# Kernel tuning notes

Measured on AMD Instinct MI355X. Metric: run time of the kernel, lower is better.

## Reference

```python
import jax, jax.numpy as jnp
import numpy as np

CHUNK = 128


def setup_inputs() -> dict:
    key = jax.random.key(0)
    ks = jax.random.split(key, 10)
    B, L, d, n = 4, 2048, 192, 64
    sd = 1.0 / np.sqrt(d)
    return {
        "x": jax.random.normal(ks[0], (B, L, d), dtype=jnp.float32),
        "A_log": -jnp.log(2.0) + 0.1 * jax.random.normal(ks[1], (d,), dtype=jnp.float32),
        "W_B": sd * jax.random.normal(ks[2], (n, d), dtype=jnp.float32),
        "W_C": sd * jax.random.normal(ks[3], (n, d), dtype=jnp.float32),
        "W_dt": sd * jax.random.normal(ks[4], (d, d), dtype=jnp.float32),
        "b_dt": 0.1 * jax.random.normal(ks[5], (d,), dtype=jnp.float32),
        "W_xp": sd * jax.random.normal(ks[6], (2 * d, d), dtype=jnp.float32),
        "b_xp": 0.1 * jax.random.normal(ks[7], (2 * d,), dtype=jnp.float32),
        "W_out": sd * jax.random.normal(ks[8], (d, d), dtype=jnp.float32),
        "b_out": 0.1 * jax.random.normal(ks[9], (d,), dtype=jnp.float32),
    }


def reference(x, A_log, W_B, W_C, W_dt, b_dt, W_xp, b_xp, W_out, b_out):
    p = CHUNK
    b, l, d = x.shape
    n = W_B.shape[0]
    pad = (-l) % p
    xp = jnp.pad(x, ((0, 0), (0, pad), (0, 0))) if pad > 0 else x
    c = xp.shape[1] // p

    A = -jnp.exp(A_log)                                   # (d,)
    proj = xp @ W_xp.T + b_xp                             # (b, Lp, 2d)
    x_bar, z = jnp.split(proj, 2, axis=-1)
    Bm = x_bar @ W_B.T                                    # (b, Lp, n)
    Cm = x_bar @ W_C.T                                    # (b, Lp, n)
    dt = jax.nn.softplus(x_bar @ W_dt.T + b_dt)           # (b, Lp, d)
    A_bar = jnp.exp(dt * A)                               # (b, Lp, d)

    resh = lambda t: t.reshape(b, c, p, t.shape[-1])
    xc, Bc, Cc, Ac = resh(x_bar), resh(Bm), resh(Cm), resh(A_bar)

    # intra-chunk: masked decay matrix M[b,c,i,j,d]
    log_A = jnp.log(jnp.abs(Ac) + 1e-8)
    la_cum = jnp.cumsum(log_A, axis=2)                    # (b,c,p,d)
    log_M = la_cum[:, :, :, None, :] - la_cum[:, :, None, :, :]
    causal = jnp.tril(jnp.ones((p, p), dtype=x.dtype))
    M = jnp.exp(log_M) * causal[None, None, :, :, None]   # (b,c,p,p,d)
    G = jnp.einsum('bcin,bcjn->bcij', Cc, Bc)             # C_i . B_j
    # same math as einsum('bcpn,bcpnd->bcpd', C, einsum('bcijd,bcjnd->bcind', M, B x))
    y_intra = jnp.einsum('bcij,bcijd,bcjd->bcid', G, M, xc)

    # inter-chunk recurrence over chunk states
    chunk_A = jnp.prod(Ac, axis=2)                        # (b,c,d)
    chunk_states = jnp.einsum('bcpn,bcpd->bcnd', Bc, xc * Ac)

    def step(state, inp):
        ca, cs = inp                                       # (b,d), (b,n,d)
        return state * ca[:, None, :] + cs, state          # emit state BEFORE update

    _, prev = jax.lax.scan(
        step,
        jnp.zeros((b, n, d), dtype=x.dtype),
        (jnp.moveaxis(chunk_A, 1, 0), jnp.moveaxis(chunk_states, 1, 0)),
    )
    prev = jnp.moveaxis(prev, 0, 1)                       # (b,c,n,d)
    y_inter = jnp.einsum('bcpn,bcnd->bcpd', Cc, prev)

    y = (y_intra + y_inter).reshape(b, c * p, d)[:, :l]
    y = y * jax.nn.silu(z[:, :l])
    return y @ W_out.T + b_out
```

## Files before the change

### kernel.cpp

```cpp
#include <hip/hip_runtime.h>
#include <math.h>

#define TOK      8192
#define DIM      192
#define NST      64
#define PCHUNK   128
#define NCHUNKS  64
#define CPB      16
#define BATCH    4
#define SUB      32
#define NSUB     4
#define NG       4
#define NPG      16

typedef __attribute__((ext_vector_type(8))) short  bf16x8;
typedef __attribute__((ext_vector_type(4))) float  f32x4;

__device__ __forceinline__ unsigned short f2bf(float f) {
    unsigned int u = __float_as_uint(f);
    u += 0x7fff + ((u >> 16) & 1);
    return (unsigned short)(u >> 16);
}
__device__ __forceinline__ float bf2f(unsigned short h) {
    return __uint_as_float(((unsigned int)h) << 16);
}

#define XU      393216
#define WXPU    18432
#define WOUTU   9216
#define CAST_U  (XU + WXPU + WOUTU)
#define FOLD_U  15360
#define PREP_N  (CAST_U + FOLD_U + 704)

__global__ __launch_bounds__(256)
void prep_kernel(const float* __restrict__ x,   const float* __restrict__ Wxp,
                 const float* __restrict__ WB,  const float* __restrict__ WC,
                 const float* __restrict__ Wdt, const float* __restrict__ Wout,
                 const float* __restrict__ b_xp, const float* __restrict__ b_dt,
                 unsigned short* __restrict__ xb,
                 unsigned short* __restrict__ bigW,
                 unsigned short* __restrict__ woutb,
                 float* __restrict__ biasAll)
{
    int u = blockIdx.x * 256 + threadIdx.x;
    if (u < CAST_U) {
        const float* src; unsigned short* dst; int idx;
        if      (u < XU)        { src = x;    dst = xb;    idx = u; }
        else if (u < XU + WXPU) { src = Wxp;  dst = bigW;  idx = u - XU; }
        else                    { src = Wout; dst = woutb; idx = u - XU - WXPU; }
        float4 v = *(const float4*)(src + (size_t)idx * 4);
        ushort4 r; r.x = f2bf(v.x); r.y = f2bf(v.y); r.z = f2bf(v.z); r.w = f2bf(v.w);
        *(ushort4*)(dst + (size_t)idx * 4) = r;
    } else if (u < CAST_U + FOLD_U) {
        int idx = u - CAST_U;
        int n = idx / 48, k4 = idx % 48;
        const float* wr = (n < 64) ? WB + (size_t)n * DIM
                        : (n < 128) ? WC + (size_t)(n - 64) * DIM
                                    : Wdt + (size_t)(n - 128) * DIM;
        float4 acc = {0.f, 0.f, 0.f, 0.f};
        for (int j = 0; j < DIM; ++j) {
            float w = wr[j];
            float4 xp = *(const float4*)(Wxp + (size_t)j * DIM + k4 * 4);
            acc.x = fmaf(w, xp.x, acc.x); acc.y = fmaf(w, xp.y, acc.y);
            acc.z = fmaf(w, xp.z, acc.z); acc.w = fmaf(w, xp.w, acc.w);
        }
        ushort4 r; r.x = f2bf(acc.x); r.y = f2bf(acc.y); r.z = f2bf(acc.z); r.w = f2bf(acc.w);
        *(ushort4*)(bigW + (size_t)(384 + n) * DIM + k4 * 4) = r;
    } else if (u < PREP_N) {
        int col = u - CAST_U - FOLD_U;
        if (col < 384) { biasAll[col] = b_xp[col]; return; }
        int n = col - 384;
        const float* wr = (n < 64) ? WB + (size_t)n * DIM
                        : (n < 128) ? WC + (size_t)(n - 64) * DIM
                                    : Wdt + (size_t)(n - 128) * DIM;
        float a0 = 0.f, a1 = 0.f, a2 = 0.f, a3 = 0.f;
        for (int j = 0; j < DIM; j += 4) {
            a0 = fmaf(wr[j+0], b_xp[j+0], a0);
            a1 = fmaf(wr[j+1], b_xp[j+1], a1);
            a2 = fmaf(wr[j+2], b_xp[j+2], a2);
            a3 = fmaf(wr[j+3], b_xp[j+3], a3);
        }
        float acc = (a0 + a1) + (a2 + a3);
        if (n >= 128) acc += b_dt[n - 128];
        biasAll[col] = acc;
    }
}

__global__ __launch_bounds__(256)
void gemm_all(const unsigned short* __restrict__ xb,
              const unsigned short* __restrict__ bigW,
              const float* __restrict__ biasAll, const float* __restrict__ A_log,
              float* __restrict__ xbar, float* __restrict__ zarr,
              float* __restrict__ BC, float* __restrict__ Abar)
{
    const int lane = threadIdx.x & 63, wave = threadIdx.x >> 6;
    const int m_wave = blockIdx.x * 128 + wave * 32;
    const int n0 = blockIdx.y * 64;
    const int lr = lane & 15, kg = lane >> 4;
    f32x4 acc[2][4] = {};
    for (int k0 = 0; k0 < DIM; k0 += 32) {
        bf16x8 af[2], bfr[4];
        #pragma unroll
        for (int mi = 0; mi < 2; ++mi)
            af[mi] = *(const bf16x8*)(xb + (size_t)(m_wave + mi*16 + lr) * DIM + k0 + kg*8);
        #pragma unroll
        for (int ni = 0; ni < 4; ++ni)
            bfr[ni] = *(const bf16x8*)(bigW + (size_t)(n0 + ni*16 + lr) * DIM + k0 + kg*8);
        #pragma unroll
        for (int mi = 0; mi < 2; ++mi)
            #pragma unroll
            for (int ni = 0; ni < 4; ++ni)
                acc[mi][ni] = __builtin_amdgcn_mfma_f32_16x16x32_bf16(
                                  af[mi], bfr[ni], acc[mi][ni], 0, 0, 0);
    }
    if (n0 < 384) {
        float* dst = (n0 < 192) ? xbar : zarr;
        int cofs = (n0 < 192) ? 0 : 192;
        #pragma unroll
        for (int ni = 0; ni < 4; ++ni) {
            int col = n0 + ni*16 + lr;
            float bias = biasAll[col];
            #pragma unroll
            for (int mi = 0; mi < 2; ++mi)
                #pragma unroll
                for (int r = 0; r < 4; ++r) {
                    int row = m_wave + mi*16 + kg*4 + r;
                    dst[(size_t)row * DIM + col - cofs] = acc[mi][ni][r] + bias;
                }
        }
    } else if (n0 < 512) {
        #pragma unroll
        for (int ni = 0; ni < 4; ++ni) {
            int col = n0 + ni*16 + lr;
            float bias = biasAll[col];
            #pragma unroll
            for (int mi = 0; mi < 2; ++mi)
                #pragma unroll
                for (int r = 0; r < 4; ++r) {
                    int row = m_wave + mi*16 + kg*4 + r;
                    BC[(size_t)row * 128 + col - 384] = acc[mi][ni][r] + bias;
                }
        }
    } else {
        #pragma unroll
        for (int ni = 0; ni < 4; ++ni) {
            int col = n0 + ni*16 + lr;
            int c2 = col - 512;
            float bias = biasAll[col];
            float Av = -expf(A_log[c2]);
            #pragma unroll
            for (int mi = 0; mi < 2; ++mi)
                #pragma unroll
                for (int r = 0; r < 4; ++r) {
                    int row = m_wave + mi*16 + kg*4 + r;
                    float v = acc[mi][ni][r] + bias;
                    float sp = (v > 20.f) ? v : log1pf(expf(v));
                    Abar[(size_t)row * DIM + c2] = expf(sp * Av);
                }
        }
    }
}

__global__ __launch_bounds__(256)
void out_gemm(const unsigned short* __restrict__ ygb,
              const unsigned short* __restrict__ woutb,
              const float* __restrict__ b_out, float* __restrict__ out)
{
    const int lane = threadIdx.x & 63, wave = threadIdx.x >> 6;
    const int m0 = blockIdx.x * 64 + wave * 16;
    const int n0 = blockIdx.y * 64;
    const int lr = lane & 15, kg = lane >> 4;
    f32x4 acc[4] = {};
    for (int k0 = 0; k0 < DIM; k0 += 32) {
        bf16x8 af = *(const bf16x8*)(ygb + (size_t)(m0 + lr) * DIM + k0 + kg*8);
        bf16x8 bfr[4];
        #pragma unroll
        for (int ni = 0; ni < 4; ++ni)
            bfr[ni] = *(const bf16x8*)(woutb + (size_t)(n0 + ni*16 + lr) * DIM + k0 + kg*8);
        #pragma unroll
        for (int ni = 0; ni < 4; ++ni)
            acc[ni] = __builtin_amdgcn_mfma_f32_16x16x32_bf16(af, bfr[ni], acc[ni], 0, 0, 0);
    }
    #pragma unroll
    for (int ni = 0; ni < 4; ++ni) {
        int col = n0 + ni*16 + lr;
        float bias = b_out[col];
        #pragma unroll
        for (int r = 0; r < 4; ++r) {
            int row = m0 + kg*4 + r;
            out[(size_t)row * DIM + col] = acc[ni][r] + bias;
        }
    }
}

__global__ __launch_bounds__(192)
void state_kernel(const float* __restrict__ xbar,
                  const float* __restrict__ Abar,
                  const float* __restrict__ Bm,
                  float* __restrict__ S,
                  float* __restrict__ R,
                  float* __restrict__ dprod)
{
    int bc = blockIdx.x, s = blockIdx.y, g = blockIdx.z;
    int dd = threadIdx.x;
    int t0 = bc * PCHUNK + s * SUB;
    __shared__ float Bs[SUB][NPG];
    if (threadIdx.x < SUB * NPG / 4) {
        int row = threadIdx.x >> 2, c4 = threadIdx.x & 3;
        *(float4*)&Bs[row][c4 * 4] =
            *(const float4*)(Bm + (size_t)(t0 + row) * 128 + g * NPG + c4 * 4);
    }
    __syncthreads();
    float H[NPG] = {}, Rr[NPG] = {};
    float cp = 1.f;
    float a_cur = Abar[(size_t)t0 * DIM + dd] + 1e-8f;
    float x_cur = xbar[(size_t)t0 * DIM + dd];
    for (int i = 0; i < SUB; ++i) {
        float a_nxt = 0.f, x_nxt = 0.f;
        if (i + 1 < SUB) {
            a_nxt = Abar[(size_t)(t0 + i + 1) * DIM + dd] + 1e-8f;
            x_nxt = xbar[(size_t)(t0 + i + 1) * DIM + dd];
        }
        cp *= a_cur;
        float4 b0 = *(const float4*)&Bs[i][0];
        float4 b1 = *(const float4*)&Bs[i][4];
        float4 b2 = *(const float4*)&Bs[i][8];
        float4 b3 = *(const float4*)&Bs[i][12];
        float bb[NPG] = {b0.x,b0.y,b0.z,b0.w, b1.x,b1.y,b1.z,b1.w,
                         b2.x,b2.y,b2.z,b2.w, b3.x,b3.y,b3.z,b3.w};
        #pragma unroll
        for (int j = 0; j < NPG; ++j) {
            float u = bb[j] * x_cur;
            H[j]  = fmaf(a_cur, H[j], u);
            Rr[j] = fmaf(u, a_cur, Rr[j]);
        }
        a_cur = a_nxt; x_cur = x_nxt;
    }
    size_t base = (((size_t)(bc * NSUB + s)) * NST + g * NPG) * DIM + dd;
    #pragma unroll
    for (int j = 0; j < NPG; ++j) {
        S[base + (size_t)j * DIM] = H[j];
        R[base + (size_t)j * DIM] = Rr[j];
    }
    if (g == 0) dprod[(size_t)(bc * NSUB + s) * DIM + dd] = cp;
}

__global__ __launch_bounds__(256)
void scan_kernel(const float* __restrict__ dprod,
                 const float* __restrict__ R,
                 float* __restrict__ prev)
{
    int v = blockIdx.x * 256 + threadIdx.x;
    if (v >= BATCH * NST * 48) return;
    int dd = (v % 48) * 4;
    int nn = (v / 48) % NST;
    int b  = v / (48 * NST);
    int bc0 = b * CPB;
    const size_t Q2 = (size_t)NST * DIM;
    float4 rv[NSUB], dv[NSUB];
    {
        size_t so = ((size_t)(bc0 * NSUB) * NST + nn) * DIM + dd;
        size_t po = (size_t)(bc0 * NSUB) * DIM + dd;
        #pragma unroll
        for (int s = 0; s < NSUB; ++s) {
            rv[s] = *(const float4*)(R + so + (size_t)s * Q2);
            dv[s] = *(const float4*)(dprod + po + (size_t)s * DIM);
        }
    }
    float4 st = {0.f, 0.f, 0.f, 0.f};
    for (int c = 0; c < CPB; ++c) {
        int bc = bc0 + c;
        float4 rn[NSUB], dn[NSUB];
        if (c + 1 < CPB) {
            size_t so = ((size_t)((bc + 1) * NSUB) * NST + nn) * DIM + dd;
            size_t po = (size_t)((bc + 1) * NSUB) * DIM + dd;
            #pragma unroll
            for (int s = 0; s < NSUB; ++s) {
                rn[s] = *(const float4*)(R + so + (size_t)s * Q2);
                dn[s] = *(const float4*)(dprod + po + (size_t)s * DIM);
            }
        }
        float4 Rs, cA;
        Rs.x = (rv[0].x + rv[1].x) + (rv[2].x + rv[3].x);
        Rs.y = (rv[0].y + rv[1].y) + (rv[2].y + rv[3].y);
        Rs.z = (rv[0].z + rv[1].z) + (rv[2].z + rv[3].z);
        Rs.w = (rv[0].w + rv[1].w) + (rv[2].w + rv[3].w);
        cA.x = (dv[0].x * dv[1].x) * (dv[2].x * dv[3].x);
        cA.y = (dv[0].y * dv[1].y) * (dv[2].y * dv[3].y);
        cA.z = (dv[0].z * dv[1].z) * (dv[2].z * dv[3].z);
        cA.w = (dv[0].w * dv[1].w) * (dv[2].w * dv[3].w);
        *(float4*)(prev + ((size_t)bc * NST + nn) * DIM + dd) = st;
        st.x = fmaf(st.x, cA.x, Rs.x);
        st.y = fmaf(st.y, cA.y, Rs.y);
        st.z = fmaf(st.z, cA.z, Rs.z);
        st.w = fmaf(st.w, cA.w, Rs.w);
        #pragma unroll
        for (int s = 0; s < NSUB; ++s) { rv[s] = rn[s]; dv[s] = dn[s]; }
    }
}

__global__ __launch_bounds__(192)
void intra_kernel(const float* __restrict__ xbar,
                  const float* __restrict__ Abar,
                  const float* __restrict__ BC,
                  const float* __restrict__ prev,
                  const float* __restrict__ S,
                  const float* __restrict__ dprod,
                  unsigned short* __restrict__ p_y)
{
    int bc = blockIdx.x, s = blockIdx.y, g = blockIdx.z;
    int dd = threadIdx.x;
    int t0 = bc * PCHUNK + s * SUB;
    __shared__ float Bs[SUB][NPG];
    __shared__ float Cs[SUB][NPG];
    {
        int nunits = SUB * NPG / 4;
        for (int idx = threadIdx.x; idx < 2 * nunits; idx += 192) {
            int m = idx >= nunits;
            int q = idx - m * nunits;
            int row = q >> 2, c4 = q & 3;
            const float* src = BC + (size_t)(t0 + row) * 128
                             + (m ? 64 : 0) + g * NPG + c4 * 4;
            float4 v = *(const float4*)src;
            if (m) *(float4*)&Cs[row][c4 * 4] = v;
            else   *(float4*)&Bs[row][c4 * 4] = v;
        }
    }
    float H[NPG] = {}, P[NPG];
    for (int k = 0; k < s; ++k) {
        float dpk = dprod[(size_t)(bc * NSUB + k) * DIM + dd];
        size_t sb = (((size_t)(bc * NSUB + k)) * NST + g * NPG) * DIM + dd;
        #pragma unroll
        for (int j = 0; j < NPG; ++j)
            H[j] = fmaf(H[j], dpk, S[sb + (size_t)j * DIM]);
    }
    #pragma unroll
    for (int j = 0; j < NPG; ++j)
        P[j] = prev[((size_t)bc * NST + g * NPG + j) * DIM + dd];
    __syncthreads();

    float a_cur = Abar[(size_t)t0 * DIM + dd] + 1e-8f;
    float x_cur = xbar[(size_t)t0 * DIM + dd];
    for (int i = 0; i < SUB; ++i) {
        int t = t0 + i;
        float a_nxt = 0.f, x_nxt = 0.f;
        if (i + 1 < SUB) {
            a_nxt = Abar[(size_t)(t + 1) * DIM + dd] + 1e-8f;
            x_nxt = xbar[(size_t)(t + 1) * DIM + dd];
        }
        float4 b0 = *(const float4*)&Bs[i][0];
        float4 b1 = *(const float4*)&Bs[i][4];
        float4 b2 = *(const float4*)&Bs[i][8];
        float4 b3 = *(const float4*)&Bs[i][12];
        float4 c0 = *(const float4*)&Cs[i][0];
        float4 c1 = *(const float4*)&Cs[i][4];
        float4 c2 = *(const float4*)&Cs[i][8];
        float4 c3 = *(const float4*)&Cs[i][12];
        float bb[NPG] = {b0.x,b0.y,b0.z,b0.w, b1.x,b1.y,b1.z,b1.w,
                         b2.x,b2.y,b2.z,b2.w, b3.x,b3.y,b3.z,b3.w};
        float cc[NPG] = {c0.x,c0.y,c0.z,c0.w, c1.x,c1.y,c1.z,c1.w,
                         c2.x,c2.y,c2.z,c2.w, c3.x,c3.y,c3.z,c3.w};
        float ya[4] = {0.f, 0.f, 0.f, 0.f};
        #pragma unroll
        for (int j = 0; j < NPG; ++j) {
            H[j] = fmaf(a_cur, H[j], bb[j] * x_cur);
            ya[j & 3] = fmaf(cc[j], H[j] + P[j], ya[j & 3]);
        }
        p_y[((size_t)g * TOK + t) * DIM + dd] = f2bf((ya[0] + ya[1]) + (ya[2] + ya[3]));
        a_cur = a_nxt; x_cur = x_nxt;
    }
}

__global__ __launch_bounds__(256)
void gate_kernel(const unsigned short* __restrict__ p_y,
                 const float* __restrict__ zarr,
                 unsigned short* __restrict__ ygb)
{
    int v = blockIdx.x * 256 + threadIdx.x;
    if (v >= TOK * 48) return;
    int t = v / 48;
    int dd = (v % 48) * 4;
    const size_t Q = (size_t)TOK * DIM;
    size_t off = (size_t)t * DIM + dd;
    float acc[4] = {0.f, 0.f, 0.f, 0.f};
    #pragma unroll
    for (int gidx = 0; gidx < NG; ++gidx) {
        ushort4 y = *(const ushort4*)(p_y + off + (size_t)gidx * Q);
        acc[0] += bf2f(y.x); acc[1] += bf2f(y.y);
        acc[2] += bf2f(y.z); acc[3] += bf2f(y.w);
    }
    float4 z = *(const float4*)(zarr + off);
    ushort4 r;
    r.x = f2bf(acc[0] * (z.x / (1.f + expf(-z.x))));
    r.y = f2bf(acc[1] * (z.y / (1.f + expf(-z.y))));
    r.z = f2bf(acc[2] * (z.z / (1.f + expf(-z.z))));
    r.w = f2bf(acc[3] * (z.w / (1.f + expf(-z.w))));
    *(ushort4*)(ygb + off) = r;
}

extern "C" void kernel_launch(void* const* d_in, const int* in_sizes, int n_in,
                              void* d_out, int out_size, void* d_ws, size_t ws_size,
                              hipStream_t stream)
{
    (void)in_sizes; (void)n_in; (void)out_size; (void)ws_size;
    const float* x     = (const float*)d_in[0];
    const float* A_log = (const float*)d_in[1];
    const float* W_B   = (const float*)d_in[2];
    const float* W_C   = (const float*)d_in[3];
    const float* W_dt  = (const float*)d_in[4];
    const float* b_dt  = (const float*)d_in[5];
    const float* W_xp  = (const float*)d_in[6];
    const float* b_xp  = (const float*)d_in[7];
    const float* W_out = (const float*)d_in[8];
    const float* b_out = (const float*)d_in[9];
    float* out = (float*)d_out;

    char* w = (char*)d_ws;
    auto take = [&](size_t bytes) { char* p = w; w += (bytes + 255) & ~(size_t)255; return p; };
    unsigned short* xb     = (unsigned short*)take((size_t)TOK*DIM*2);
    unsigned short* bigW   = (unsigned short*)take((size_t)704*DIM*2);
    unsigned short* woutb  = (unsigned short*)take((size_t)DIM*DIM*2);
    float*          biasAll= (float*)         take((size_t)704*4);
    float*          xbar   = (float*)         take((size_t)TOK*DIM*4);
    float*          zarr   = (float*)         take((size_t)TOK*DIM*4);
    float*          BC     = (float*)         take((size_t)TOK*128*4);
    float*          Abar   = (float*)         take((size_t)TOK*DIM*4);
    float*          dprod  = (float*)         take((size_t)NCHUNKS*NSUB*DIM*4);
    float*          prev   = (float*)         take((size_t)NCHUNKS*NST*DIM*4);
    float*          Sarr   = (float*)         take((size_t)NCHUNKS*NSUB*NST*DIM*4);
    float*          Rarr   = (float*)         take((size_t)NCHUNKS*NSUB*NST*DIM*4);
    unsigned short* p_y    = (unsigned short*)take((size_t)NG*TOK*DIM*2);
    unsigned short* ygb    = (unsigned short*)take((size_t)TOK*DIM*2);

    dim3 blk(256);

    prep_kernel<<<dim3((PREP_N + 255)/256), blk, 0, stream>>>(
        x, W_xp, W_B, W_C, W_dt, W_out, b_xp, b_dt, xb, bigW, woutb, biasAll);
    gemm_all<<<dim3(TOK/128, 704/64), blk, 0, stream>>>(
        xb, bigW, biasAll, A_log, xbar, zarr, BC, Abar);
    state_kernel<<<dim3(NCHUNKS, NSUB, NG), dim3(192), 0, stream>>>(
        xbar, Abar, BC, Sarr, Rarr, dprod);
    scan_kernel<<<dim3((BATCH*NST*48 + 255)/256), blk, 0, stream>>>(dprod, Rarr, prev);
    intra_kernel<<<dim3(NCHUNKS, NSUB, NG), dim3(192), 0, stream>>>(
        xbar, Abar, BC, prev, Sarr, dprod, p_y);
    gate_kernel<<<dim3((TOK*48 + 255)/256), blk, 0, stream>>>(p_y, zarr, ygb);
    out_gemm<<<dim3(TOK/64, DIM/64), blk, 0, stream>>>(ygb, woutb, b_out, out);
}
```

Baseline: 177.4 us.

## Store xbar, z and Abar in bf16, halve sub-chunk length, shrink gemm tile

The projection GEMM now writes x_bar, z and A_bar as bf16 instead of fp32, which halves the intermediate traffic read by the state, intra and gate kernels. Sub-chunks shrink from 32 to 16 steps (8 per chunk) to double parallelism in the sequential state and intra kernels. The scan kernel is simplified to load per-chunk partials inline, and the gemm tile is halved to launch more blocks. Storing A_bar in bf16 risks accuracy loss in cumulative decay products, and the larger NSUB adds more partial states to write and reduce.

```diff
diff --git a/kernel.cpp b/kernel.cpp
--- a/kernel.cpp
+++ b/kernel.cpp
@@ -8,8 +8,8 @@
 #define NCHUNKS  64
 #define CPB      16
 #define BATCH    4
-#define SUB      32
-#define NSUB     4
+#define SUB      16
+#define NSUB     8
 #define NG       4
 #define NPG      16
 
@@ -90,43 +90,36 @@
 void gemm_all(const unsigned short* __restrict__ xb,
               const unsigned short* __restrict__ bigW,
               const float* __restrict__ biasAll, const float* __restrict__ A_log,
-              float* __restrict__ xbar, float* __restrict__ zarr,
-              float* __restrict__ BC, float* __restrict__ Abar)
+              unsigned short* __restrict__ xbarb, unsigned short* __restrict__ zarrb,
+              float* __restrict__ BC, unsigned short* __restrict__ Abarb)
 {
     const int lane = threadIdx.x & 63, wave = threadIdx.x >> 6;
-    const int m_wave = blockIdx.x * 128 + wave * 32;
+    const int m0 = blockIdx.x * 64 + wave * 16;
     const int n0 = blockIdx.y * 64;
     const int lr = lane & 15, kg = lane >> 4;
-    f32x4 acc[2][4] = {};
+    f32x4 acc[4] = {};
     for (int k0 = 0; k0 < DIM; k0 += 32) {
-        bf16x8 af[2], bfr[4];
-        #pragma unroll
-        for (int mi = 0; mi < 2; ++mi)
-            af[mi] = *(const bf16x8*)(xb + (size_t)(m_wave + mi*16 + lr) * DIM + k0 + kg*8);
+        bf16x8 af = *(const bf16x8*)(xb + (size_t)(m0 + lr) * DIM + k0 + kg*8);
+        bf16x8 bfr[4];
         #pragma unroll
         for (int ni = 0; ni < 4; ++ni)
             bfr[ni] = *(const bf16x8*)(bigW + (size_t)(n0 + ni*16 + lr) * DIM + k0 + kg*8);
         #pragma unroll
-        for (int mi = 0; mi < 2; ++mi)
-            #pragma unroll
-            for (int ni = 0; ni < 4; ++ni)
-                acc[mi][ni] = __builtin_amdgcn_mfma_f32_16x16x32_bf16(
-                                  af[mi], bfr[ni], acc[mi][ni], 0, 0, 0);
+        for (int ni = 0; ni < 4; ++ni)
+            acc[ni] = __builtin_amdgcn_mfma_f32_16x16x32_bf16(af, bfr[ni], acc[ni], 0, 0, 0);
     }
     if (n0 < 384) {
-        float* dst = (n0 < 192) ? xbar : zarr;
+        unsigned short* dst = (n0 < 192) ? xbarb : zarrb;
         int cofs = (n0 < 192) ? 0 : 192;
         #pragma unroll
         for (int ni = 0; ni < 4; ++ni) {
             int col = n0 + ni*16 + lr;
             float bias = biasAll[col];
             #pragma unroll
-            for (int mi = 0; mi < 2; ++mi)
-                #pragma unroll
-                for (int r = 0; r < 4; ++r) {
-                    int row = m_wave + mi*16 + kg*4 + r;
-                    dst[(size_t)row * DIM + col - cofs] = acc[mi][ni][r] + bias;
-                }
+            for (int r = 0; r < 4; ++r) {
+                int row = m0 + kg*4 + r;
+                dst[(size_t)row * DIM + col - cofs] = f2bf(acc[ni][r] + bias);
+            }
         }
     } else if (n0 < 512) {
         #pragma unroll
@@ -134,12 +127,10 @@
             int col = n0 + ni*16 + lr;
             float bias = biasAll[col];
             #pragma unroll
-            for (int mi = 0; mi < 2; ++mi)
-                #pragma unroll
-                for (int r = 0; r < 4; ++r) {
-                    int row = m_wave + mi*16 + kg*4 + r;
-                    BC[(size_t)row * 128 + col - 384] = acc[mi][ni][r] + bias;
-                }
+            for (int r = 0; r < 4; ++r) {
+                int row = m0 + kg*4 + r;
+                BC[(size_t)row * 128 + col - 384] = acc[ni][r] + bias;
+            }
         }
     } else {
         #pragma unroll
@@ -149,14 +140,12 @@
             float bias = biasAll[col];
             float Av = -expf(A_log[c2]);
             #pragma unroll
-            for (int mi = 0; mi < 2; ++mi)
-                #pragma unroll
-                for (int r = 0; r < 4; ++r) {
-                    int row = m_wave + mi*16 + kg*4 + r;
-                    float v = acc[mi][ni][r] + bias;
-                    float sp = (v > 20.f) ? v : log1pf(expf(v));
-                    Abar[(size_t)row * DIM + c2] = expf(sp * Av);
-                }
+            for (int r = 0; r < 4; ++r) {
+                int row = m0 + kg*4 + r;
+                float v = acc[ni][r] + bias;
+                float sp = (v > 20.f) ? v : log1pf(expf(v));
+                Abarb[(size_t)row * DIM + c2] = f2bf(expf(sp * Av));
+            }
         }
     }
 }
@@ -194,8 +183,8 @@
 }
 
 __global__ __launch_bounds__(192)
-void state_kernel(const float* __restrict__ xbar,
-                  const float* __restrict__ Abar,
+void state_kernel(const unsigned short* __restrict__ xbarb,
+                  const unsigned short* __restrict__ Abarb,
                   const float* __restrict__ Bm,
                   float* __restrict__ S,
                   float* __restrict__ R,
@@ -213,13 +202,13 @@
     __syncthreads();
     float H[NPG] = {}, Rr[NPG] = {};
     float cp = 1.f;
-    float a_cur = Abar[(size_t)t0 * DIM + dd] + 1e-8f;
-    float x_cur = xbar[(size_t)t0 * DIM + dd];
+    float a_cur = bf2f(Abarb[(size_t)t0 * DIM + dd]) + 1e-8f;
+    float x_cur = bf2f(xbarb[(size_t)t0 * DIM + dd]);
     for (int i = 0; i < SUB; ++i) {
         float a_nxt = 0.f, x_nxt = 0.f;
         if (i + 1 < SUB) {
-            a_nxt = Abar[(size_t)(t0 + i + 1) * DIM + dd] + 1e-8f;
-            x_nxt = xbar[(size_t)(t0 + i + 1) * DIM + dd];
+            a_nxt = bf2f(Abarb[(size_t)(t0 + i + 1) * DIM + dd]) + 1e-8f;
+            x_nxt = bf2f(xbarb[(size_t)(t0 + i + 1) * DIM + dd]);
         }
         cp *= a_cur;
         float4 b0 = *(const float4*)&Bs[i][0];
@@ -257,51 +246,31 @@
     int b  = v / (48 * NST);
     int bc0 = b * CPB;
     const size_t Q2 = (size_t)NST * DIM;
-    float4 rv[NSUB], dv[NSUB];
-    {
-        size_t so = ((size_t)(bc0 * NSUB) * NST + nn) * DIM + dd;
-        size_t po = (size_t)(bc0 * NSUB) * DIM + dd;
-        #pragma unroll
-        for (int s = 0; s < NSUB; ++s) {
-            rv[s] = *(const float4*)(R + so + (size_t)s * Q2);
-            dv[s] = *(const float4*)(dprod + po + (size_t)s * DIM);
-        }
-    }
     float4 st = {0.f, 0.f, 0.f, 0.f};
     for (int c = 0; c < CPB; ++c) {
         int bc = bc0 + c;
-        float4 rn[NSUB], dn[NSUB];
-        if (c + 1 < CPB) {
-            size_t so = ((size_t)((bc + 1) * NSUB) * NST + nn) * DIM + dd;
-            size_t po = (size_t)((bc + 1) * NSUB) * DIM + dd;
-            #pragma unroll
-            for (int s = 0; s < NSUB; ++s) {
-                rn[s] = *(const float4*)(R + so + (size_t)s * Q2);
-                dn[s] = *(const float4*)(dprod + po + (size_t)s * DIM);
-            }
-        }
-        float4 Rs, cA;
-        Rs.x = (rv[0].x + rv[1].x) + (rv[2].x + rv[3].x);
-        Rs.y = (rv[0].y + rv[1].y) + (rv[2].y + rv[3].y);
-        Rs.z = (rv[0].z + rv[1].z) + (rv[2].z + rv[3].z);
-        Rs.w = (rv[0].w + rv[1].w) + (rv[2].w + rv[3].w);
-        cA.x = (dv[0].x * dv[1].x) * (dv[2].x * dv[3].x);
-        cA.y = (dv[0].y * dv[1].y) * (dv[2].y * dv[3].y);
-        cA.z = (dv[0].z * dv[1].z) * (dv[2].z * dv[3].z);
-        cA.w = (dv[0].w * dv[1].w) * (dv[2].w * dv[3].w);
+        size_t so = ((size_t)(bc * NSUB) * NST + nn) * DIM + dd;
+        size_t po = (size_t)(bc * NSUB) * DIM + dd;
+        float4 Rs = {0.f, 0.f, 0.f, 0.f};
+        float4 cA = {1.f, 1.f, 1.f, 1.f};
+        #pragma unroll
+        for (int s = 0; s < NSUB; ++s) {
+            float4 rv = *(const float4*)(R + so + (size_t)s * Q2);
+            float4 dv = *(const float4*)(dprod + po + (size_t)s * DIM);
+            Rs.x += rv.x; Rs.y += rv.y; Rs.z += rv.z; Rs.w += rv.w;
+            cA.x *= dv.x; cA.y *= dv.y; cA.z *= dv.z; cA.w *= dv.w;
+        }
         *(float4*)(prev + ((size_t)bc * NST + nn) * DIM + dd) = st;
         st.x = fmaf(st.x, cA.x, Rs.x);
         st.y = fmaf(st.y, cA.y, Rs.y);
         st.z = fmaf(st.z, cA.z, Rs.z);
         st.w = fmaf(st.w, cA.w, Rs.w);
-        #pragma unroll
-        for (int s = 0; s < NSUB; ++s) { rv[s] = rn[s]; dv[s] = dn[s]; }
     }
 }
 
 __global__ __launch_bounds__(192)
-void intra_kernel(const float* __restrict__ xbar,
-                  const float* __restrict__ Abar,
+void intra_kernel(const unsigned short* __restrict__ xbarb,
+                  const unsigned short* __restrict__ Abarb,
                   const float* __restrict__ BC,
                   const float* __restrict__ prev,
                   const float* __restrict__ S,
@@ -339,14 +308,14 @@
         P[j] = prev[((size_t)bc * NST + g * NPG + j) * DIM + dd];
     __syncthreads();
 
-    float a_cur = Abar[(size_t)t0 * DIM + dd] + 1e-8f;
-    float x_cur = xbar[(size_t)t0 * DIM + dd];
+    float a_cur = bf2f(Abarb[(size_t)t0 * DIM + dd]) + 1e-8f;
+    float x_cur = bf2f(xbarb[(size_t)t0 * DIM + dd]);
     for (int i = 0; i < SUB; ++i) {
         int t = t0 + i;
         float a_nxt = 0.f, x_nxt = 0.f;
         if (i + 1 < SUB) {
-            a_nxt = Abar[(size_t)(t + 1) * DIM + dd] + 1e-8f;
-            x_nxt = xbar[(size_t)(t + 1) * DIM + dd];
+            a_nxt = bf2f(Abarb[(size_t)(t + 1) * DIM + dd]) + 1e-8f;
+            x_nxt = bf2f(xbarb[(size_t)(t + 1) * DIM + dd]);
         }
         float4 b0 = *(const float4*)&Bs[i][0];
         float4 b1 = *(const float4*)&Bs[i][4];
@@ -373,7 +342,7 @@
 
 __global__ __launch_bounds__(256)
 void gate_kernel(const unsigned short* __restrict__ p_y,
-                 const float* __restrict__ zarr,
+                 const unsigned short* __restrict__ zarrb,
                  unsigned short* __restrict__ ygb)
 {
     int v = blockIdx.x * 256 + threadIdx.x;
@@ -389,12 +358,13 @@
         acc[0] += bf2f(y.x); acc[1] += bf2f(y.y);
         acc[2] += bf2f(y.z); acc[3] += bf2f(y.w);
     }
-    float4 z = *(const float4*)(zarr + off);
+    ushort4 zu = *(const ushort4*)(zarrb + off);
+    float z0 = bf2f(zu.x), z1 = bf2f(zu.y), z2 = bf2f(zu.z), z3 = bf2f(zu.w);
     ushort4 r;
-    r.x = f2bf(acc[0] * (z.x / (1.f + expf(-z.x))));
-    r.y = f2bf(acc[1] * (z.y / (1.f + expf(-z.y))));
-    r.z = f2bf(acc[2] * (z.z / (1.f + expf(-z.z))));
-    r.w = f2bf(acc[3] * (z.w / (1.f + expf(-z.w))));
+    r.x = f2bf(acc[0] * (z0 / (1.f + expf(-z0))));
+    r.y = f2bf(acc[1] * (z1 / (1.f + expf(-z1))));
+    r.z = f2bf(acc[2] * (z2 / (1.f + expf(-z2))));
+    r.w = f2bf(acc[3] * (z3 / (1.f + expf(-z3))));
     *(ushort4*)(ygb + off) = r;
 }
 
@@ -421,10 +391,10 @@
     unsigned short* bigW   = (unsigned short*)take((size_t)704*DIM*2);
     unsigned short* woutb  = (unsigned short*)take((size_t)DIM*DIM*2);
     float*          biasAll= (float*)         take((size_t)704*4);
-    float*          xbar   = (float*)         take((size_t)TOK*DIM*4);
-    float*          zarr   = (float*)         take((size_t)TOK*DIM*4);
+    unsigned short* xbarb  = (unsigned short*)take((size_t)TOK*DIM*2);
+    unsigned short* zarrb  = (unsigned short*)take((size_t)TOK*DIM*2);
     float*          BC     = (float*)         take((size_t)TOK*128*4);
-    float*          Abar   = (float*)         take((size_t)TOK*DIM*4);
+    unsigned short* Abarb  = (unsigned short*)take((size_t)TOK*DIM*2);
     float*          dprod  = (float*)         take((size_t)NCHUNKS*NSUB*DIM*4);
     float*          prev   = (float*)         take((size_t)NCHUNKS*NST*DIM*4);
     float*          Sarr   = (float*)         take((size_t)NCHUNKS*NSUB*NST*DIM*4);
@@ -436,13 +406,13 @@
 
     prep_kernel<<<dim3((PREP_N + 255)/256), blk, 0, stream>>>(
         x, W_xp, W_B, W_C, W_dt, W_out, b_xp, b_dt, xb, bigW, woutb, biasAll);
-    gemm_all<<<dim3(TOK/128, 704/64), blk, 0, stream>>>(
-        xb, bigW, biasAll, A_log, xbar, zarr, BC, Abar);
+    gemm_all<<<dim3(TOK/64, 704/64), blk, 0, stream>>>(
+        xb, bigW, biasAll, A_log, xbarb, zarrb, BC, Abarb);
     state_kernel<<<dim3(NCHUNKS, NSUB, NG), dim3(192), 0, stream>>>(
-        xbar, Abar, BC, Sarr, Rarr, dprod);
+        xbarb, Abarb, BC, Sarr, Rarr, dprod);
     scan_kernel<<<dim3((BATCH*NST*48 + 255)/256), blk, 0, stream>>>(dprod, Rarr, prev);
     intra_kernel<<<dim3(NCHUNKS, NSUB, NG), dim3(192), 0, stream>>>(
-        xbar, Abar, BC, prev, Sarr, dprod, p_y);
-    gate_kernel<<<dim3((TOK*48 + 255)/256), blk, 0, stream>>>(p_y, zarr, ygb);
+        xbarb, Abarb, BC, prev, Sarr, dprod, p_y);
+    gate_kernel<<<dim3((TOK*48 + 255)/256), blk, 0, stream>>>(p_y, zarrb, ygb);
     out_gemm<<<dim3(TOK/64, DIM/64), blk, 0, stream>>>(ygb, woutb, b_out, out);
 }
```

After: 193.5 us. 1.09x slower.
